# Optimization experiments

Hardware: AMD Instinct MI355X
Metric: run time of the kernel (lower is better)

The kernel has to match this reference:

```python
import jax, jax.numpy as jnp
import numpy as np

T, B, TD, HD, VD = 64, 4096, 512, 256, 484
LN_EPS = 1e-5   # torch nn.LayerNorm default
COS_EPS = 1e-8  # torch F.cosine_similarity default


def setup_inputs() -> dict:
    key = jax.random.key(0)
    ks = jax.random.split(key, 6)
    w = lambda k, shape: jax.random.normal(k, shape, dtype=jnp.float32) * 0.02
    return {
        "t_feat": jax.random.normal(ks[0], (B, TD), dtype=jnp.float32),
        "W1": w(ks[1], (T, HD, TD)),            # torch Linear weight layout [out, in]
        "b1": w(ks[2], (T, HD)),
        "gamma": jnp.ones((T, HD), jnp.float32),
        "beta": jnp.zeros((T, HD), jnp.float32),
        "W2": w(ks[3], (T, VD, HD)),
        "b2": w(ks[4], (T, VD)),
        "centroids": jax.random.normal(ks[5], (T, VD), dtype=jnp.float32),
    }


def reference(t_feat, W1, b1, gamma, beta, W2, b2, centroids):
    # All T per-task mappers batched into one grouped GEMM pipeline.
    # Linear1: [B, TD] x [T, HD, TD] -> [T, B, HD]
    h = jnp.einsum("bd,thd->tbh", t_feat, W1) + b1[:, None, :]
    # LayerNorm over hidden dim (per task affine params)
    mu = jnp.mean(h, axis=-1, keepdims=True)
    var = jnp.mean(jnp.square(h - mu), axis=-1, keepdims=True)
    h = (h - mu) * jax.lax.rsqrt(var + LN_EPS) * gamma[:, None, :] + beta[:, None, :]
    # Exact GELU (torch nn.GELU default uses erf)
    h = jax.nn.gelu(h, approximate=False)
    # Linear2: [T, B, HD] x [T, VD, HD] -> [T, B, VD] predicted visual features
    v = jnp.einsum("tbh,tvh->tbv", h, W2) + b2[:, None, :]
    # Cosine similarity vs each task centroid (eps-clamped norms, as in torch)
    v_norm = jnp.maximum(jnp.linalg.norm(v, axis=-1), COS_EPS)          # [T, B]
    c_norm = jnp.maximum(jnp.linalg.norm(centroids, axis=-1), COS_EPS)  # [T]
    cos = jnp.einsum("tbv,tv->tb", v, centroids) / (v_norm * c_norm[:, None])
    distances = jnp.mean(1.0 - cos, axis=-1)  # [T] mean cosine distance per task
    best_task = jnp.argmin(distances)          # top-1 routing decision
    return distances, best_task
```

## Files before the change

kernel.cpp:

```cpp
#include <hip/hip_runtime.h>
#include <math.h>

#define TASKS 64
#define NB    4096
#define TDI   512
#define HDI   256
#define VDI   484

#define WS_TF   ((size_t)0)
#define WS_W1   ((size_t)4194304)
#define WS_W2   ((size_t)20971520)
#define WS_CN   ((size_t)37748736)
#define WS_BC   ((size_t)37748992)
#define WS_ACC  ((size_t)37749248)
#define WS_WCP  ((size_t)37749504)

#define LDS_HP 0
#define LDS_B2 32768
#define LDS_R0 34816
#define LDS_R1 35840
#define LDS_MU 36864
#define LDS_RS 37120
#define SMEM_BYTES 37376

typedef _Float16 half8 __attribute__((ext_vector_type(8)));
typedef float    f32x4 __attribute__((ext_vector_type(4)));

#define MFMA16(a, b, c) __builtin_amdgcn_mfma_f32_16x16x32_f16((a), (b), (c), 0, 0, 0)

__device__ __forceinline__ void gld_lds16(const void* g, void* l) {
  __builtin_amdgcn_global_load_lds((const __attribute__((address_space(1))) void*)g,
                                   (__attribute__((address_space(3))) void*)l, 16, 0, 0);
}

__device__ __forceinline__ float gelu_exact(float x) {
  float az = fabsf(x) * 0.70710678118654752f;
  float d  = fmaf(0.3275911f, az, 1.0f);
  float t; asm("v_rcp_f32 %0, %1" : "=v"(t) : "v"(d));
  float p  = fmaf(t, 1.061405429f, -1.453152027f);
  p = fmaf(t, p, 1.421413741f);
  p = fmaf(t, p, -0.284496736f);
  p = fmaf(t, p, 0.254829592f);
  p = p * t;
  float m = az * az * -1.4426950408889634f;
  float e; asm("v_exp_f32 %0, %1" : "=v"(e) : "v"(m));
  float er = fmaf(-p, e, 1.0f);
  er = copysignf(er, x);
  float hx = 0.5f * x;
  return fmaf(hx, er, hx);
}

extern "C" __global__ void __launch_bounds__(256, 8)
prep_all(const float* __restrict__ t_feat,
         const float* __restrict__ W1,
         const float* __restrict__ W2,
         const float* __restrict__ cent,
         _Float16* __restrict__ tf,
         _Float16* __restrict__ w1,
         _Float16* __restrict__ w2,
         float* __restrict__ wcp) {
  __shared__ __align__(16) char pbuf[17408];
  const int bid = blockIdx.x, tid = threadIdx.x;

  const float* src;
  half8* dst;
  int w2vdBase = -1;
  int wcSlot = 0, tTask = 0;

  if (bid < 256) {
    int g = bid;
    int rb = g >> 2, kq = g & 3;
    src = t_feat + (size_t)rb * 64 * 512 + kq * 128;
    dst = (half8*)tf + ((size_t)rb * 4096 + kq * 1024);
  } else if (bid < 1280) {
    int g = bid - 256;
    int t = g >> 4, w_ = (g >> 2) & 3, kq = g & 3;
    src = W1 + ((size_t)t * 256 + w_ * 64) * 512 + kq * 128;
    dst = (half8*)w1 + ((size_t)t * 16384 + w_ * 4096 + kq * 1024);
  } else {
    int g = bid - 1280;
    int t = g >> 4, sub = g & 15;
    int p = sub >> 3, w_ = (sub >> 1) & 3, kq = sub & 1;
    src = W2 + (size_t)t * 484 * 256 + kq * 128;
    w2vdBase = p * 256 + w_ * 64;
    dst = (half8*)w2 + ((size_t)t * 16384 + p * 8192 + w_ * 2048 + kq * 1024);
    wcSlot = (p * 4 + w_) * 2 + kq;
    tTask = t;
  }

  const int srcStride = (w2vdBase < 0) ? 512 : 256;
  ushort* lds = (ushort*)pbuf;
  f32x4 psum = {0.f, 0.f, 0.f, 0.f};
  #pragma unroll
  for (int j = 0; j < 8; ++j) {
    int f = j * 256 + tid;
    int row = f >> 5, kc = f & 31;
    f32x4 v0 = {0.f, 0.f, 0.f, 0.f};
    if (w2vdBase < 0) {
      v0 = __builtin_nontemporal_load(((const f32x4*)(src + (size_t)row * srcStride)) + kc);
    } else {
      int vd = w2vdBase + row;
      if (vd < VDI) {
        v0 = __builtin_nontemporal_load(((const f32x4*)(src + (size_t)vd * 256)) + kc);
        float cv = cent[(size_t)tTask * VDI + vd];
        psum += v0 * cv;
      }
    }
    _Float16 h4[4] = {(_Float16)v0[0], (_Float16)v0[1], (_Float16)v0[2], (_Float16)v0[3]};
    *(ushort4*)(&lds[row * 136 + kc * 4]) = *(const ushort4*)h4;
  }
  __syncthreads();

  #pragma unroll
  for (int j = 0; j < 4; ++j) {
    int u = j * 256 + tid;
    int ksl = u >> 8, rg = (u >> 6) & 3, q = (u >> 4) & 3, l15 = u & 15;
    int row = rg * 16 + l15, k8l = ksl * 4 + q;
    half8 val = *(const half8*)(pbuf + row * 272 + k8l * 16);
    __builtin_nontemporal_store(val, dst + u);
  }

  if (w2vdBase >= 0) {
    __syncthreads();
    ((f32x4*)pbuf)[(tid >> 5) * 32 + (tid & 31)] = psum;
    __syncthreads();
    if (tid < 128) {
      const float* ps = (const float*)pbuf;
      float s = 0.f;
      #pragma unroll
      for (int ro = 0; ro < 8; ++ro) s += ps[ro * 128 + tid];
      __builtin_nontemporal_store(s, wcp + ((size_t)tTask * 16 + wcSlot) * 128 + tid);
    }
  }
}

extern "C" __global__ void prep_fin(const float* __restrict__ wcp,
                                    const float* __restrict__ b2,
                                    const float* __restrict__ cent,
                                    _Float16* __restrict__ w2,
                                    float* __restrict__ cnorm,
                                    float* __restrict__ bc,
                                    float* __restrict__ accum) {
  __shared__ float redc[256], redb[256];
  const int t = blockIdx.x, h = threadIdx.x;
  int kq = h >> 7, h128 = h & 127;
  float wc = 0.f;
  #pragma unroll
  for (int pg = 0; pg < 8; ++pg)
    wc += __builtin_nontemporal_load(wcp + ((size_t)t * 16 + pg * 2 + kq) * 128 + h128);
  int ks = h >> 5, q = (h >> 3) & 3;
  size_t o = (size_t)t * 16384 + 8192 + 3 * 2048 + ks * 256 + 2 * 64 + q * 16 + 4;
  __builtin_nontemporal_store((_Float16)wc, w2 + o * 8 + (h & 7));

  float c2 = 0.f, b2c = 0.f;
  for (int v = h; v < VDI; v += 256) {
    float c = cent[(size_t)t * VDI + v];
    c2 += c * c;
    b2c += b2[(size_t)t * VDI + v] * c;
  }
  redc[h] = c2; redb[h] = b2c;
  __syncthreads();
  if (h < 64) {
    c2  = redc[h] + redc[h + 64] + redc[h + 128] + redc[h + 192];
    b2c = redb[h] + redb[h + 64] + redb[h + 128] + redb[h + 192];
    #pragma unroll
    for (int off = 32; off; off >>= 1) { c2 += __shfl_xor(c2, off); b2c += __shfl_xor(b2c, off); }
    if (h == 0) { cnorm[t] = sqrtf(c2); bc[t] = b2c; accum[t] = 0.f; }
  }
}


#define STEP_AB(ACC, PBP, HN) do {                                             \
  __builtin_amdgcn_s_setprio(1);                                               \
  ACC[0][0]=MFMA16(a0[0],b[0],ACC[0][0]); ACC[1][0]=MFMA16(a0[1],b[0],ACC[1][0]); \
  ACC[2][0]=MFMA16(a0[2],b[0],ACC[2][0]); ACC[3][0]=MFMA16(a0[3],b[0],ACC[3][0]); \
  b[0]=(PBP)[0];                                                               \
  ACC[0][1]=MFMA16(a0[0],b[1],ACC[0][1]); ACC[1][1]=MFMA16(a0[1],b[1],ACC[1][1]); \
  ACC[2][1]=MFMA16(a0[2],b[1],ACC[2][1]); ACC[3][1]=MFMA16(a0[3],b[1],ACC[3][1]); \
  b[1]=(PBP)[64];                                                              \
  ACC[0][2]=MFMA16(a0[0],b[2],ACC[0][2]); ACC[1][2]=MFMA16(a0[1],b[2],ACC[1][2]); \
  ACC[2][2]=MFMA16(a0[2],b[2],ACC[2][2]); ACC[3][2]=MFMA16(a0[3],b[2],ACC[3][2]); \
  b[2]=(PBP)[128];                                                             \
  ACC[0][3]=MFMA16(a0[0],b[3],ACC[0][3]); a0[0]=*(const half8*)(HN);           \
  ACC[1][3]=MFMA16(a0[1],b[3],ACC[1][3]); a0[1]=*(const half8*)((HN)+1024);    \
  ACC[2][3]=MFMA16(a0[2],b[3],ACC[2][3]); a0[2]=*(const half8*)((HN)+2048);    \
  ACC[3][3]=MFMA16(a0[3],b[3],ACC[3][3]); a0[3]=*(const half8*)((HN)+3072);    \
  b[3]=(PBP)[192]; (PBP)+=256;                                                 \
  __builtin_amdgcn_s_setprio(0);                                               \
} while (0)

#define STEP_BO(ACC, PBP) do {                                                 \
  __builtin_amdgcn_s_setprio(1);                                               \
  _Pragma("unroll") for (int ct_ = 0; ct_ < 4; ++ct_) {                        \
    ACC[0][ct_] = MFMA16(a0[0], b[ct_], ACC[0][ct_]);                          \
    ACC[1][ct_] = MFMA16(a0[1], b[ct_], ACC[1][ct_]);                          \
    ACC[2][ct_] = MFMA16(a0[2], b[ct_], ACC[2][ct_]);                          \
    ACC[3][ct_] = MFMA16(a0[3], b[ct_], ACC[3][ct_]);                          \
    b[ct_] = (PBP)[ct_ * 64];                                                  \
  }                                                                            \
  (PBP) += 256;                                                                \
  __builtin_amdgcn_s_setprio(0);                                               \
} while (0)

#define STEP_LAST(ACC) do {                                                    \
  __builtin_amdgcn_s_setprio(1);                                               \
  _Pragma("unroll") for (int ct_ = 0; ct_ < 4; ++ct_) {                        \
    ACC[0][ct_] = MFMA16(a0[0], b[ct_], ACC[0][ct_]);                          \
    ACC[1][ct_] = MFMA16(a0[1], b[ct_], ACC[1][ct_]);                          \
    ACC[2][ct_] = MFMA16(a0[2], b[ct_], ACC[2][ct_]);                          \
    ACC[3][ct_] = MFMA16(a0[3], b[ct_], ACC[3][ct_]);                          \
  }                                                                            \
  __builtin_amdgcn_s_setprio(0);                                               \
} while (0)

#define LD_A4L(D, P) do {                                                      \
  D[0] = *(const half8*)(P);        D[1] = *(const half8*)((P) + 1024);        \
  D[2] = *(const half8*)((P) + 2048); D[3] = *(const half8*)((P) + 3072); } while (0)

#define STAGE_A(Q, BUF) do {                                                   \
  const half8* gs_ = gA + (Q) * 1024 + tid;                                    \
  char* lb_ = (BUF) + (size_t)w * 1024;                                        \
  gld_lds16(gs_,       lb_);                                                   \
  gld_lds16(gs_ + 256, lb_ + 4096);                                            \
  gld_lds16(gs_ + 512, lb_ + 8192);                                            \
  gld_lds16(gs_ + 768, lb_ + 12288);                                           \
} while (0)

extern "C" __global__ void __launch_bounds__(256, 4)
router_main(const half8* __restrict__ tfv,
            const half8* __restrict__ w1v,
            const half8* __restrict__ w2v,
            const float* __restrict__ b1,
            const float* __restrict__ gamma,
            const float* __restrict__ beta,
            const float* __restrict__ b2,
            const float* __restrict__ bc,
            const float* __restrict__ cnorm,
            float* __restrict__ accum) {
  __shared__ __align__(16) char smem[SMEM_BYTES];

  const int tid = threadIdx.x;
  const int bx  = blockIdx.x;
  const int t  = ((bx & 7) << 3) | (bx >> 9);
  const int rb = (bx >> 3) & 63;

  const int lane = tid & 63;
  const int w    = tid >> 6;
  const int quad = lane >> 4;
  const int l15  = lane & 15;

  f32x4 zero4 = {0.f, 0.f, 0.f, 0.f};
  f32x4 acc[4][4];
  #pragma unroll
  for (int rt = 0; rt < 4; ++rt)
    #pragma unroll
    for (int ct = 0; ct < 4; ++ct) acc[rt][ct] = zero4;

  half8 a0[4], b[4];

  {
    const half8* gA = tfv + (size_t)rb * 4096;
    char* buf0 = smem + LDS_HP;
    char* buf1 = smem + LDS_HP + 16384;
    const half8* pb = w1v + ((size_t)t * 16384 + w * 4096 + quad * 16 + l15);
    const char* hav0 = buf0 + quad * 256 + l15 * 16;
    const char* hav1 = buf1 + quad * 256 + l15 * 16;

    STAGE_A(0, buf0);
    STAGE_A(1, buf1);
    b[0] = pb[0]; b[1] = pb[64]; b[2] = pb[128]; b[3] = pb[192]; pb += 256;
    __syncthreads();

    LD_A4L(a0, hav0);
    STEP_AB(acc, pb, hav0 + 4096);
    STEP_AB(acc, pb, hav0 + 8192);
    STEP_AB(acc, pb, hav0 + 12288);
    STEP_BO(acc, pb);
    __syncthreads();
    STAGE_A(2, buf0);
    LD_A4L(a0, hav1);
    STEP_AB(acc, pb, hav1 + 4096);
    STEP_AB(acc, pb, hav1 + 8192);
    STEP_AB(acc, pb, hav1 + 12288);
    STEP_BO(acc, pb);
    __syncthreads();
    STAGE_A(3, buf1);
    LD_A4L(a0, hav0);
    STEP_AB(acc, pb, hav0 + 4096);
    STEP_AB(acc, pb, hav0 + 8192);
    STEP_AB(acc, pb, hav0 + 12288);
    STEP_BO(acc, pb);
    __syncthreads();
    LD_A4L(a0, hav1);
    STEP_AB(acc, pb, hav1 + 4096);
    STEP_AB(acc, pb, hav1 + 8192);
    STEP_AB(acc, pb, hav1 + 12288);
    STEP_LAST(acc);
  }

  float b1v[4];
  #pragma unroll
  for (int ct = 0; ct < 4; ++ct)
    b1v[ct] = b1[t * HDI + w * 64 + ct * 16 + l15];
  {
    float* red0 = (float*)(smem + LDS_R0);
    float* red1 = (float*)(smem + LDS_R1);
    #pragma unroll
    for (int rt = 0; rt < 4; ++rt)
      #pragma unroll
      for (int r = 0; r < 4; ++r) {
        float sv = 0.f, qv = 0.f;
        #pragma unroll
        for (int ct = 0; ct < 4; ++ct) {
          float v = acc[rt][ct][r] + b1v[ct];
          acc[rt][ct][r] = v;
          sv += v; qv += v * v;
        }
        sv += __shfl_xor(sv, 1); qv += __shfl_xor(qv, 1);
        sv += __shfl_xor(sv, 2); qv += __shfl_xor(qv, 2);
        sv += __shfl_xor(sv, 4); qv += __shfl_xor(qv, 4);
        sv += __shfl_xor(sv, 8); qv += __shfl_xor(qv, 8);
        if (l15 == 0) {
          int m = rt * 16 + quad * 4 + r;
          red0[w * 64 + m] = sv;
          red1[w * 64 + m] = qv;
        }
      }
    __syncthreads();
    if (tid < 64) {
      float s = red0[tid] + red0[64 + tid] + red0[128 + tid] + red0[192 + tid];
      float q = red1[tid] + red1[64 + tid] + red1[128 + tid] + red1[192 + tid];
      float mu = s * (1.f / HDI);
      float var = q * (1.f / HDI) - mu * mu;
      ((float*)(smem + LDS_MU))[tid] = mu;
      ((float*)(smem + LDS_RS))[tid] = rsqrtf(var + 1e-5f);
    }
    float gvv[4], bevv[4];
    #pragma unroll
    for (int ct = 0; ct < 4; ++ct) {
      gvv[ct]  = gamma[t * HDI + w * 64 + ct * 16 + l15];
      bevv[ct] = beta [t * HDI + w * 64 + ct * 16 + l15];
    }
    {
      float* b2s = (float*)(smem + LDS_B2);
      int i0 = tid;
      b2s[i0] = (i0 < VDI) ? b2[(size_t)t * VDI + i0] : 0.f;
      int i1 = tid + 256;
      float v = 0.f;
      if (i1 < VDI) v = b2[(size_t)t * VDI + i1];
      else if (i1 == VDI) v = bc[t];
      b2s[i1] = v;
    }
    __syncthreads();
    const float* mus = (const float*)(smem + LDS_MU);
    const float* rss = (const float*)(smem + LDS_RS);
    #pragma unroll
    for (int rt = 0; rt < 4; ++rt) {
      float m4[4], s4[4];
      #pragma unroll
      for (int r = 0; r < 4; ++r) {
        int m = rt * 16 + quad * 4 + r;
        m4[r] = mus[m]; s4[r] = rss[m];
      }
      #pragma unroll
      for (int ct = 0; ct < 4; ++ct) {
        int col = w * 64 + ct * 16 + l15;
        int base = (((col >> 5) * 4 + rt) * 4 + ((col >> 3) & 3)) * 256
                 + quad * 64 + (l15 & 7) * 2;
        #pragma unroll
        for (int r = 0; r < 4; ++r) {
          float x = (acc[rt][ct][r] - m4[r]) * s4[r];
          x = x * gvv[ct] + bevv[ct];
          *(_Float16*)(smem + LDS_HP + base + r * 16) = (_Float16)gelu_exact(x);
        }
      }
    }
    __syncthreads();
  }

  {
    const float* b2s = (const float*)(smem + LDS_B2);
    float* red0 = (float*)(smem + LDS_R0);
    float* red1 = (float*)(smem + LDS_R1);
    const char* ha = smem + LDS_HP + quad * 256 + l15 * 16;

    #pragma unroll 1
    for (int pass = 0; pass < 2; ++pass) {
      const half8* pc = w2v + ((size_t)t * 16384 + pass * 8192 + w * 2048 + quad * 16 + l15);
      f32x4 acc2[4][4];
      #pragma unroll
      for (int rt = 0; rt < 4; ++rt)
        #pragma unroll
        for (int ct = 0; ct < 4; ++ct) acc2[rt][ct] = zero4;

      LD_A4L(a0, ha);
      b[0] = pc[0]; b[1] = pc[64]; b[2] = pc[128]; b[3] = pc[192];
      pc += 256;
      #pragma unroll 1
      for (int ks = 0; ks < 7; ++ks) {
        STEP_AB(acc2, pc, ha + (ks + 1) * 4096);
      }
      STEP_LAST(acc2);

      float bv[4];
      #pragma unroll
      for (int ct = 0; ct < 4; ++ct)
        bv[ct] = b2s[pass * 256 + w * 64 + ct * 16 + l15];
      #pragma unroll
      for (int rt = 0; rt < 4; ++rt)
        #pragma unroll
        for (int r = 0; r < 4; ++r) {
          float ssq = 0.f;
          #pragma unroll
          for (int ct = 0; ct < 4; ++ct) {
            int vcol = pass * 256 + w * 64 + ct * 16 + l15;
            float val = acc2[rt][ct][r] + bv[ct];
            ssq += (vcol < VDI) ? val * val : 0.f;
          }
          ssq += __shfl_xor(ssq, 1);
          ssq += __shfl_xor(ssq, 2);
          ssq += __shfl_xor(ssq, 4);
          ssq += __shfl_xor(ssq, 8);
          int m = rt * 16 + quad * 4 + r;
          if (l15 == 0) {
            if (pass == 0) red0[w * 64 + m] = ssq;
            else           red0[w * 64 + m] += ssq;
          }
          if (pass == 1 && w == 3 && l15 == 4)
            red1[192 + m] = acc2[rt][2][r] + bv[2];
        }
    }

    __syncthreads();
    if (tid < 64) {
      float ss  = red0[tid] + red0[64 + tid] + red0[128 + tid] + red0[192 + tid];
      float dot = red1[192 + tid];
      float cn = fmaxf(cnorm[t], 1e-8f);
      float vn = fmaxf(sqrtf(ss), 1e-8f);
      float part = 1.0f - dot / (vn * cn);
      part += __shfl_down(part, 32);
      part += __shfl_down(part, 16);
      part += __shfl_down(part, 8);
      part += __shfl_down(part, 4);
      part += __shfl_down(part, 2);
      part += __shfl_down(part, 1);
      if (tid == 0) atomicAdd(accum + t, part);
    }
  }
}

extern "C" __global__ void finalize_k(const float* __restrict__ accum, float* __restrict__ out) {
  int t = threadIdx.x;
  float d = accum[t] * (1.0f / (float)NB);
  out[t] = d;
  float bd = d; int bi = t;
  #pragma unroll
  for (int off = 32; off; off >>= 1) {
    float od = __shfl_xor(bd, off);
    int   oi = __shfl_xor(bi, off);
    if (od < bd || (od == bd && oi < bi)) { bd = od; bi = oi; }
  }
  if (t == 0) out[64] = (float)bi;
}

extern "C" void kernel_launch(void* const* d_in, const int* in_sizes, int n_in,
                              void* d_out, int out_size, void* d_ws, size_t ws_size,
                              hipStream_t stream) {
  const float* t_feat = (const float*)d_in[0];
  const float* W1     = (const float*)d_in[1];
  const float* b1     = (const float*)d_in[2];
  const float* gamma  = (const float*)d_in[3];
  const float* beta   = (const float*)d_in[4];
  const float* W2     = (const float*)d_in[5];
  const float* b2     = (const float*)d_in[6];
  const float* cent   = (const float*)d_in[7];

  char* ws = (char*)d_ws;
  _Float16* tf = (_Float16*)(ws + WS_TF);
  _Float16* w1 = (_Float16*)(ws + WS_W1);
  _Float16* w2 = (_Float16*)(ws + WS_W2);
  float* cnorm = (float*)(ws + WS_CN);
  float* bc    = (float*)(ws + WS_BC);
  float* accum = (float*)(ws + WS_ACC);
  float* wcp   = (float*)(ws + WS_WCP);
  float* out = (float*)d_out;

  prep_all<<<2304, 256, 0, stream>>>(t_feat, W1, W2, cent, tf, w1, w2, wcp);
  prep_fin<<<64, 256, 0, stream>>>(wcp, b2, cent, w2, cnorm, bc, accum);
  router_main<<<4096, 256, 0, stream>>>((const half8*)tf, (const half8*)w1, (const half8*)w2,
                                        b1, gamma, beta, b2, bc, cnorm, accum);
  finalize_k<<<1, 64, 0, stream>>>(accum, out);
}
```

Measured before the change: 324.1 us.

## Double-buffer weight fragments two steps ahead and prefetch W2 during LayerNorm

Adds a second set of B-operand registers so the weight loads for W1 and W2 are issued two k-steps ahead instead of one, which deepens the global-load latency hiding. The first W2 fragments are prefetched during the LayerNorm/GELU epilogue, and the second pass's fragments are loaded before the first pass's epilogue. It also fully unrolls the W2 k-loop and overlaps the A-fragment reload across the first barrier. The extra registers force launch bounds to drop from 4 to 3 blocks per SM, lowering occupancy.

```diff
diff --git a/kernel.cpp b/kernel.cpp
--- a/kernel.cpp
+++ b/kernel.cpp
@@ -170,52 +170,59 @@
 }
 
 
-#define STEP_AB(ACC, PBP, HN) do {                                             \
+#define MFMA4(ACC, CT, BV)                                                     \
+  ACC[0][CT]=MFMA16(a0[0],(BV),ACC[0][CT]); ACC[1][CT]=MFMA16(a0[1],(BV),ACC[1][CT]); \
+  ACC[2][CT]=MFMA16(a0[2],(BV),ACC[2][CT]); ACC[3][CT]=MFMA16(a0[3],(BV),ACC[3][CT]);
+
+#define STEP_D2(ACC, BX, PBN, HN) do {                                         \
   __builtin_amdgcn_s_setprio(1);                                               \
-  ACC[0][0]=MFMA16(a0[0],b[0],ACC[0][0]); ACC[1][0]=MFMA16(a0[1],b[0],ACC[1][0]); \
-  ACC[2][0]=MFMA16(a0[2],b[0],ACC[2][0]); ACC[3][0]=MFMA16(a0[3],b[0],ACC[3][0]); \
-  b[0]=(PBP)[0];                                                               \
-  ACC[0][1]=MFMA16(a0[0],b[1],ACC[0][1]); ACC[1][1]=MFMA16(a0[1],b[1],ACC[1][1]); \
-  ACC[2][1]=MFMA16(a0[2],b[1],ACC[2][1]); ACC[3][1]=MFMA16(a0[3],b[1],ACC[3][1]); \
-  b[1]=(PBP)[64];                                                              \
-  ACC[0][2]=MFMA16(a0[0],b[2],ACC[0][2]); ACC[1][2]=MFMA16(a0[1],b[2],ACC[1][2]); \
-  ACC[2][2]=MFMA16(a0[2],b[2],ACC[2][2]); ACC[3][2]=MFMA16(a0[3],b[2],ACC[3][2]); \
-  b[2]=(PBP)[128];                                                             \
-  ACC[0][3]=MFMA16(a0[0],b[3],ACC[0][3]); a0[0]=*(const half8*)(HN);           \
-  ACC[1][3]=MFMA16(a0[1],b[3],ACC[1][3]); a0[1]=*(const half8*)((HN)+1024);    \
-  ACC[2][3]=MFMA16(a0[2],b[3],ACC[2][3]); a0[2]=*(const half8*)((HN)+2048);    \
-  ACC[3][3]=MFMA16(a0[3],b[3],ACC[3][3]); a0[3]=*(const half8*)((HN)+3072);    \
-  b[3]=(PBP)[192]; (PBP)+=256;                                                 \
+  MFMA4(ACC, 0, BX[0]); BX[0]=(PBN)[0];                                        \
+  MFMA4(ACC, 1, BX[1]); BX[1]=(PBN)[64];                                       \
+  MFMA4(ACC, 2, BX[2]); BX[2]=(PBN)[128];                                      \
+  ACC[0][3]=MFMA16(a0[0],BX[3],ACC[0][3]); a0[0]=*(const half8*)(HN);          \
+  ACC[1][3]=MFMA16(a0[1],BX[3],ACC[1][3]); a0[1]=*(const half8*)((HN)+1024);   \
+  ACC[2][3]=MFMA16(a0[2],BX[3],ACC[2][3]); a0[2]=*(const half8*)((HN)+2048);   \
+  ACC[3][3]=MFMA16(a0[3],BX[3],ACC[3][3]); a0[3]=*(const half8*)((HN)+3072);   \
+  BX[3]=(PBN)[192]; (PBN)+=256;                                                \
   __builtin_amdgcn_s_setprio(0);                                               \
 } while (0)
 
-#define STEP_BO(ACC, PBP) do {                                                 \
+#define STEP_D2_NA(ACC, BX, PBN) do {                                          \
   __builtin_amdgcn_s_setprio(1);                                               \
-  _Pragma("unroll") for (int ct_ = 0; ct_ < 4; ++ct_) {                        \
-    ACC[0][ct_] = MFMA16(a0[0], b[ct_], ACC[0][ct_]);                          \
-    ACC[1][ct_] = MFMA16(a0[1], b[ct_], ACC[1][ct_]);                          \
-    ACC[2][ct_] = MFMA16(a0[2], b[ct_], ACC[2][ct_]);                          \
-    ACC[3][ct_] = MFMA16(a0[3], b[ct_], ACC[3][ct_]);                          \
-    b[ct_] = (PBP)[ct_ * 64];                                                  \
-  }                                                                            \
-  (PBP) += 256;                                                                \
+  MFMA4(ACC, 0, BX[0]); BX[0]=(PBN)[0];                                        \
+  MFMA4(ACC, 1, BX[1]); BX[1]=(PBN)[64];                                       \
+  MFMA4(ACC, 2, BX[2]); BX[2]=(PBN)[128];                                      \
+  MFMA4(ACC, 3, BX[3]); BX[3]=(PBN)[192];                                      \
+  (PBN)+=256;                                                                  \
   __builtin_amdgcn_s_setprio(0);                                               \
 } while (0)
 
-#define STEP_LAST(ACC) do {                                                    \
+#define STEP_D2_NB(ACC, BX, HN) do {                                           \
   __builtin_amdgcn_s_setprio(1);                                               \
-  _Pragma("unroll") for (int ct_ = 0; ct_ < 4; ++ct_) {                        \
-    ACC[0][ct_] = MFMA16(a0[0], b[ct_], ACC[0][ct_]);                          \
-    ACC[1][ct_] = MFMA16(a0[1], b[ct_], ACC[1][ct_]);                          \
-    ACC[2][ct_] = MFMA16(a0[2], b[ct_], ACC[2][ct_]);                          \
-    ACC[3][ct_] = MFMA16(a0[3], b[ct_], ACC[3][ct_]);                          \
-  }                                                                            \
+  MFMA4(ACC, 0, BX[0]);                                                        \
+  MFMA4(ACC, 1, BX[1]);                                                        \
+  MFMA4(ACC, 2, BX[2]);                                                        \
+  ACC[0][3]=MFMA16(a0[0],BX[3],ACC[0][3]); a0[0]=*(const half8*)(HN);          \
+  ACC[1][3]=MFMA16(a0[1],BX[3],ACC[1][3]); a0[1]=*(const half8*)((HN)+1024);   \
+  ACC[2][3]=MFMA16(a0[2],BX[3],ACC[2][3]); a0[2]=*(const half8*)((HN)+2048);   \
+  ACC[3][3]=MFMA16(a0[3],BX[3],ACC[3][3]); a0[3]=*(const half8*)((HN)+3072);   \
+  __builtin_amdgcn_s_setprio(0);                                               \
+} while (0)
+
+#define STEP_LAST(ACC, BX) do {                                                \
+  __builtin_amdgcn_s_setprio(1);                                               \
+  MFMA4(ACC, 0, BX[0]);                                                        \
+  MFMA4(ACC, 1, BX[1]);                                                        \
+  MFMA4(ACC, 2, BX[2]);                                                        \
+  MFMA4(ACC, 3, BX[3]);                                                        \
   __builtin_amdgcn_s_setprio(0);                                               \
 } while (0)
 
 #define LD_A4L(D, P) do {                                                      \
   D[0] = *(const half8*)(P);        D[1] = *(const half8*)((P) + 1024);        \
   D[2] = *(const half8*)((P) + 2048); D[3] = *(const half8*)((P) + 3072); } while (0)
+
+#define LD_B4(D, P) do { D[0]=(P)[0]; D[1]=(P)[64]; D[2]=(P)[128]; D[3]=(P)[192]; } while (0)
 
 #define STAGE_A(Q, BUF) do {                                                   \
   const half8* gs_ = gA + (Q) * 1024 + tid;                                    \
@@ -226,7 +233,7 @@
   gld_lds16(gs_ + 768, lb_ + 12288);                                           \
 } while (0)
 
-extern "C" __global__ void __launch_bounds__(256, 4)
+extern "C" __global__ void __launch_bounds__(256, 3)
 router_main(const half8* __restrict__ tfv,
             const half8* __restrict__ w1v,
             const half8* __restrict__ w2v,
@@ -256,7 +263,7 @@
     #pragma unroll
     for (int ct = 0; ct < 4; ++ct) acc[rt][ct] = zero4;
 
-  half8 a0[4], b[4];
+  half8 a0[4], bA[4], bB[4];
 
   {
     const half8* gA = tfv + (size_t)rb * 4096;
@@ -268,34 +275,35 @@
 
     STAGE_A(0, buf0);
     STAGE_A(1, buf1);
-    b[0] = pb[0]; b[1] = pb[64]; b[2] = pb[128]; b[3] = pb[192]; pb += 256;
+    LD_B4(bA, pb);
+    LD_B4(bB, (pb + 256));
+    const half8* pbn = pb + 512;
     __syncthreads();
 
     LD_A4L(a0, hav0);
-    STEP_AB(acc, pb, hav0 + 4096);
-    STEP_AB(acc, pb, hav0 + 8192);
-    STEP_AB(acc, pb, hav0 + 12288);
-    STEP_BO(acc, pb);
+    STEP_D2(acc, bA, pbn, hav0 + 4096);
+    STEP_D2(acc, bB, pbn, hav0 + 8192);
+    STEP_D2(acc, bA, pbn, hav0 + 12288);
+    STEP_D2(acc, bB, pbn, hav1);
     __syncthreads();
     STAGE_A(2, buf0);
-    LD_A4L(a0, hav1);
-    STEP_AB(acc, pb, hav1 + 4096);
-    STEP_AB(acc, pb, hav1 + 8192);
-    STEP_AB(acc, pb, hav1 + 12288);
-    STEP_BO(acc, pb);
+    STEP_D2(acc, bA, pbn, hav1 + 4096);
+    STEP_D2(acc, bB, pbn, hav1 + 8192);
+    STEP_D2(acc, bA, pbn, hav1 + 12288);
+    STEP_D2_NA(acc, bB, pbn);
     __syncthreads();
     STAGE_A(3, buf1);
     LD_A4L(a0, hav0);
-    STEP_AB(acc, pb, hav0 + 4096);
-    STEP_AB(acc, pb, hav0 + 8192);
-    STEP_AB(acc, pb, hav0 + 12288);
-    STEP_BO(acc, pb);
+    STEP_D2(acc, bA, pbn, hav0 + 4096);
+    STEP_D2(acc, bB, pbn, hav0 + 8192);
+    STEP_D2(acc, bA, pbn, hav0 + 12288);
+    STEP_D2_NA(acc, bB, pbn);
     __syncthreads();
     LD_A4L(a0, hav1);
-    STEP_AB(acc, pb, hav1 + 4096);
-    STEP_AB(acc, pb, hav1 + 8192);
-    STEP_AB(acc, pb, hav1 + 12288);
-    STEP_LAST(acc);
+    STEP_D2(acc, bA, pbn, hav1 + 4096);
+    STEP_D2(acc, bB, pbn, hav1 + 8192);
+    STEP_D2_NB(acc, bA, hav1 + 12288);
+    STEP_LAST(acc, bB);
   }
 
   float b1v[4];
@@ -352,6 +360,11 @@
       b2s[i1] = v;
     }
     __syncthreads();
+    {
+      const half8* pc0 = w2v + ((size_t)t * 16384 + w * 2048 + quad * 16 + l15);
+      LD_B4(bA, pc0);
+      LD_B4(bB, (pc0 + 256));
+    }
     const float* mus = (const float*)(smem + LDS_MU);
     const float* rss = (const float*)(smem + LDS_RS);
     #pragma unroll
@@ -383,10 +396,11 @@
     float* red0 = (float*)(smem + LDS_R0);
     float* red1 = (float*)(smem + LDS_R1);
     const char* ha = smem + LDS_HP + quad * 256 + l15 * 16;
+    const half8* pc0 = w2v + ((size_t)t * 16384 + w * 2048 + quad * 16 + l15);
 
     #pragma unroll 1
     for (int pass = 0; pass < 2; ++pass) {
-      const half8* pc = w2v + ((size_t)t * 16384 + pass * 8192 + w * 2048 + quad * 16 + l15);
+      const half8* pcn = pc0 + pass * 8192 + 512;
       f32x4 acc2[4][4];
       #pragma unroll
       for (int rt = 0; rt < 4; ++rt)
@@ -394,13 +408,18 @@
         for (int ct = 0; ct < 4; ++ct) acc2[rt][ct] = zero4;
 
       LD_A4L(a0, ha);
-      b[0] = pc[0]; b[1] = pc[64]; b[2] = pc[128]; b[3] = pc[192];
-      pc += 256;
-      #pragma unroll 1
-      for (int ks = 0; ks < 7; ++ks) {
-        STEP_AB(acc2, pc, ha + (ks + 1) * 4096);
+      STEP_D2(acc2, bA, pcn, ha + 4096);
+      STEP_D2(acc2, bB, pcn, ha + 8192);
+      STEP_D2(acc2, bA, pcn, ha + 12288);
+      STEP_D2(acc2, bB, pcn, ha + 16384);
+      STEP_D2(acc2, bA, pcn, ha + 20480);
+      STEP_D2(acc2, bB, pcn, ha + 24576);
+      STEP_D2_NB(acc2, bA, ha + 28672);
+      STEP_LAST(acc2, bB);
+      if (pass == 0) {
+        LD_B4(bA, (pc0 + 8192));
+        LD_B4(bB, (pc0 + 8192 + 256));
       }
-      STEP_LAST(acc2);
 
       float bv[4];
       #pragma unroll
```

Measured after the change: 385.8 us. 19.0% more time.
